# Optimization experiments

Measured on AMD Instinct MI355X. Metric: run time of the kernel, lower is better.

Reference implementation:

```python
import jax, jax.numpy as jnp
import numpy as np

N = 100000      # nodes
E = 1600000     # directed edges (avg degree 16)
D_IN = 64
D_OUT = 64


def setup_inputs() -> dict:
    key = jax.random.key(0)
    k1, k2, k3, k4, k5 = jax.random.split(key, 5)
    x = jax.random.normal(k1, (N, D_IN), dtype=jnp.float32)
    edge_index = jax.random.randint(k2, (2, E), 0, N, dtype=jnp.int32)
    s_in = 1.0 / np.sqrt(D_IN)
    W_conv = jax.random.normal(k3, (D_IN, D_OUT), dtype=jnp.float32) * s_in
    b_conv = jnp.zeros((D_OUT,), dtype=jnp.float32)
    W_self = jax.random.normal(k4, (D_IN, D_OUT), dtype=jnp.float32) * s_in
    b_self = jax.random.normal(k5, (D_OUT,), dtype=jnp.float32) * s_in
    return {"x": x, "edge_index": edge_index, "W_conv": W_conv, "b_conv": b_conv,
            "W_self": W_self, "b_self": b_self, "n1": 400, "n2": 250}


def reference(x, edge_index, W_conv, b_conv, W_self, b_self, n1, n2):
    # GCNConv (PyG defaults): add self-loops, symmetric normalization,
    # out_i = sum_j norm_ij * (x_j @ W_conv) + b_conv; then self-loop linear + residual.
    n = x.shape[0]
    loops = jnp.arange(n, dtype=edge_index.dtype)
    row = jnp.concatenate([edge_index[0], loops])  # source nodes [E+N]
    col = jnp.concatenate([edge_index[1], loops])  # target nodes [E+N]
    deg = jax.ops.segment_sum(jnp.ones_like(col, dtype=x.dtype), col, num_segments=n)
    dinv = jnp.where(deg > 0, jax.lax.rsqrt(deg), 0.0)      # deg^{-1/2}
    norm = dinv[row] * dinv[col]                            # [E+N]
    xw = x @ W_conv                                         # [N, D_OUT]
    msg = xw[row] * norm[:, None]                           # gather + scale [E+N, D_OUT]
    x_neigh = jax.ops.segment_sum(msg, col, num_segments=n) + b_conv
    x_self = x @ W_self + b_self
    return x_self + x_neigh
```

## Files before the change

kernel.cpp:

```cpp
#include <hip/hip_runtime.h>

#define CAP 64
#define CHUNK 4096
#define NBINS_MAX 1024
#define CAPB 2560

typedef __attribute__((ext_vector_type(8))) short bf16x8;
typedef __attribute__((ext_vector_type(4))) float f32x4;

__device__ __forceinline__ unsigned short f2bf_rne(float f) {
    unsigned u = __builtin_bit_cast(unsigned, f);
    u += 0x7FFFu + ((u >> 16) & 1u);
    return (unsigned short)(u >> 16);
}
__device__ __forceinline__ float bf2f(unsigned short h) {
    return __builtin_bit_cast(float, (unsigned)h << 16);
}


__global__ void k_zero2(int* __restrict__ gcur, int nbins, int* __restrict__ degovf,
                        int n, int* __restrict__ ovfc,
                        const float* __restrict__ Wc, const float* __restrict__ Ws,
                        unsigned short* __restrict__ bfrag) {
    const int t = threadIdx.x;
    if (blockIdx.x == gridDim.x - 1) {
        for (int s = t; s < 2048; s += 256) {
            int lane = s & 63;
            int ct   = (s >> 6) & 3;
            int ks   = (s >> 8) & 1;
            int half = (s >> 9) & 1;
            int mat  = (s >> 10) & 1;
            const float* W = mat ? Ws : Wc;
            int d = ct * 16 + (lane & 15);
            int kbase = ks * 32 + (lane >> 4) * 8;
#pragma unroll
            for (int j = 0; j < 8; ++j) {
                float v = W[(kbase + j) * 64 + d];
                unsigned u = __builtin_bit_cast(unsigned, v);
                unsigned short hi = (unsigned short)(u >> 16);
                unsigned short elem;
                if (half == 0) {
                    elem = hi;
                } else {
                    float fh = __builtin_bit_cast(float, (unsigned)hi << 16);
                    float fl = v - fh;
                    elem = (unsigned short)(__builtin_bit_cast(unsigned, fl) >> 16);
                }
                bfrag[(size_t)s * 8 + j] = elem;
            }
        }
        return;
    }
    int i = blockIdx.x * blockDim.x + t;
    if (i < nbins) gcur[i] = 0;
    if (i < n) degovf[i] = 0;
    if (i == 0) *ovfc = 0;
}

__global__ __launch_bounds__(512) void k_bin(
    const int* __restrict__ row, const int* __restrict__ col, int e, int nbins,
    int* __restrict__ gcur, unsigned int* __restrict__ records,
    int* __restrict__ degovf, int* __restrict__ ovf, int* __restrict__ ovfc)
{
    __shared__ int hist[NBINS_MAX];
    __shared__ int lofs[NBINS_MAX];
    __shared__ int gadj[NBINS_MAX];
    __shared__ int tscan[512];
    __shared__ unsigned int stage[CHUNK];
    __shared__ unsigned short sbin[CHUNK];

    const int t = threadIdx.x;
    const int base = blockIdx.x * CHUNK;
    int cnt = e - base; if (cnt > CHUNK) cnt = CHUNK;
    if (cnt <= 0) return;

    for (int i = t; i < nbins; i += 512) hist[i] = 0;
    __syncthreads();

    for (int k = t; k < cnt; k += 512) atomicAdd(&hist[col[base + k] >> 7], 1);
    __syncthreads();

    const int b0 = t * 2;
    int h0 = (b0 < nbins) ? hist[b0] : 0;
    int h1 = (b0 + 1 < nbins) ? hist[b0 + 1] : 0;
    int s = h0 + h1;
    tscan[t] = s;
    __syncthreads();
    for (int off = 1; off < 512; off <<= 1) {
        int v = (t >= off) ? tscan[t - off] : 0;
        __syncthreads();
        tscan[t] += v;
        __syncthreads();
    }
    const int tbase = tscan[t] - s;

    if (b0 < nbins) {
        int gb = h0 ? atomicAdd(&gcur[b0], h0) : 0;
        lofs[b0] = tbase; gadj[b0] = gb - tbase;
    }
    if (b0 + 1 < nbins) {
        int lb = tbase + h0;
        int gb = h1 ? atomicAdd(&gcur[b0 + 1], h1) : 0;
        lofs[b0 + 1] = lb; gadj[b0 + 1] = gb - lb;
    }
    __syncthreads();

    for (int k = t; k < cnt; k += 512) {
        int c = col[base + k];
        int r = row[base + k];
        int b = c >> 7;
        int slot = atomicAdd(&lofs[b], 1);
        stage[slot] = ((unsigned)r << 7) | (unsigned)(c & 127);
        sbin[slot] = (unsigned short)b;
    }
    __syncthreads();

    for (int k = t; k < cnt; k += 512) {
        unsigned rec = stage[k];
        int b = sbin[k];
        int g = gadj[b] + k;
        if (g < CAPB) {
            records[(size_t)b * CAPB + g] = rec;
        } else {
            int q = atomicAdd(ovfc, 1);
            int c = (b << 7) | (int)(rec & 127u);
            ovf[2 * q]     = (int)(rec >> 7);
            ovf[2 * q + 1] = c;
            atomicAdd(&degovf[c], 1);
        }
    }
}

__global__ __launch_bounds__(256) void k_dinv(
    const int* __restrict__ gcur, const unsigned int* __restrict__ records,
    const int* __restrict__ degovf, float* __restrict__ dinv, int n)
{
    __shared__ int lh[128];
    const int b = blockIdx.x, t = threadIdx.x;
    if (t < 128) lh[t] = 0;
    __syncthreads();
    int m = gcur[b]; if (m > CAPB) m = CAPB;
    const unsigned int* rb = records + (size_t)b * CAPB;
    for (int k = t; k < m; k += 256) atomicAdd(&lh[rb[k] & 127u], 1);
    __syncthreads();
    if (t < 128) {
        int node = (b << 7) + t;
        if (node < n) dinv[node] = rsqrtf((float)(lh[t] + degovf[node] + 1));
    }
}

__global__ __launch_bounds__(256) void k_gemm5(
    const float* __restrict__ x, const unsigned short* __restrict__ bfrag,
    const float* __restrict__ bc, const float* __restrict__ bs,
    const float* __restrict__ dinv, unsigned short* __restrict__ ybf,
    float* __restrict__ out, int n)
{
    const int t = threadIdx.x;
    const int lane = t & 63;
    const int wid = t >> 6;
    const int rt0 = blockIdx.x * 128 + wid * 32;
    if (rt0 >= n) return;

    const int arow = lane & 15;
    const int kgrp = lane >> 4;

    bf16x8 a_hi[2][2], a_lo[2][2];
#pragma unroll
    for (int rt = 0; rt < 2; ++rt) {
        int row = rt0 + rt * 16 + arow;
        if (row >= n) row = n - 1;
        const float* xp = x + (size_t)row * 64 + kgrp * 8;
#pragma unroll
        for (int ks = 0; ks < 2; ++ks) {
            float4 f0 = *(const float4*)(xp + ks * 32);
            float4 f1 = *(const float4*)(xp + ks * 32 + 4);
            float f[8] = {f0.x, f0.y, f0.z, f0.w, f1.x, f1.y, f1.z, f1.w};
            bf16x8 h, l;
#pragma unroll
            for (int j = 0; j < 8; ++j) {
                unsigned u = __builtin_bit_cast(unsigned, f[j]);
                unsigned short hj = (unsigned short)(u >> 16);
                float fh = __builtin_bit_cast(float, (unsigned)hj << 16);
                float fl = f[j] - fh;
                unsigned short lj = (unsigned short)(__builtin_bit_cast(unsigned, fl) >> 16);
                h[j] = (short)hj;
                l[j] = (short)lj;
            }
            a_hi[rt][ks] = h;
            a_lo[rt][ks] = l;
        }
    }

    f32x4 acc[2][2][4];
#pragma unroll
    for (int m = 0; m < 2; ++m)
#pragma unroll
        for (int rt = 0; rt < 2; ++rt)
#pragma unroll
            for (int ct = 0; ct < 4; ++ct)
                acc[m][rt][ct] = (f32x4){0.f, 0.f, 0.f, 0.f};

#pragma unroll
    for (int mat = 0; mat < 2; ++mat) {
#pragma unroll
        for (int ks = 0; ks < 2; ++ks) {
#pragma unroll
            for (int ct = 0; ct < 4; ++ct) {
                const bf16x8 bh = *(const bf16x8*)(bfrag + ((size_t)((((mat * 2 + 0) * 2 + ks) * 4 + ct) * 64 + lane)) * 8);
                const bf16x8 bl = *(const bf16x8*)(bfrag + ((size_t)((((mat * 2 + 1) * 2 + ks) * 4 + ct) * 64 + lane)) * 8);
#pragma unroll
                for (int rt = 0; rt < 2; ++rt) {
                    acc[mat][rt][ct] = __builtin_amdgcn_mfma_f32_16x16x32_bf16(a_hi[rt][ks], bh, acc[mat][rt][ct], 0, 0, 0);
                    acc[mat][rt][ct] = __builtin_amdgcn_mfma_f32_16x16x32_bf16(a_lo[rt][ks], bh, acc[mat][rt][ct], 0, 0, 0);
                    acc[mat][rt][ct] = __builtin_amdgcn_mfma_f32_16x16x32_bf16(a_hi[rt][ks], bl, acc[mat][rt][ct], 0, 0, 0);
                }
            }
        }
    }

    const int dcol = lane & 15;
    const int rbase = (lane >> 4) * 4;
    float di[2][4];
#pragma unroll
    for (int rt = 0; rt < 2; ++rt)
#pragma unroll
        for (int reg = 0; reg < 4; ++reg) {
            int row = rt0 + rt * 16 + rbase + reg;
            di[rt][reg] = dinv[(row < n) ? row : (n - 1)];
        }

#pragma unroll
    for (int ct = 0; ct < 4; ++ct) {
        int d = ct * 16 + dcol;
        float bias = bc[d] + bs[d];
#pragma unroll
        for (int rt = 0; rt < 2; ++rt) {
#pragma unroll
            for (int reg = 0; reg < 4; ++reg) {
                int row = rt0 + rt * 16 + rbase + reg;
                if (row < n) {
                    float dv = di[rt][reg];
                    float zc = acc[0][rt][ct][reg];
                    ybf[(size_t)row * 64 + d] = f2bf_rne(zc * dv);
                    out[(size_t)row * 64 + d] = acc[1][rt][ct][reg] + bias + dv * dv * zc;
                }
            }
        }
    }
}

__global__ __launch_bounds__(512) void k_gather_bin4(
    const int* __restrict__ gcur, const unsigned int* __restrict__ records,
    const unsigned short* __restrict__ ybf, const float* __restrict__ dinv,
    float* __restrict__ out, int n)
{
    __shared__ unsigned int srec[CAPB];
    __shared__ int slist[CAPB];
    __shared__ int scnt[128];
    __shared__ int sinc[128];
    __shared__ int scur[128];

    const int b = blockIdx.x, t = threadIdx.x;
    int m = gcur[b]; if (m > CAPB) m = CAPB;

    if (t < 128) scnt[t] = 0;
    __syncthreads();

    for (int k = t; k < m; k += 512) {
        unsigned r = __builtin_nontemporal_load(&records[(size_t)b * CAPB + k]);
        srec[k] = r;
        atomicAdd(&scnt[r & 127u], 1);
    }
    __syncthreads();

    if (t < 128) sinc[t] = scnt[t];
    __syncthreads();
    for (int off = 1; off < 128; off <<= 1) {
        int v = 0;
        if (t < 128 && t >= off) v = sinc[t - off];
        __syncthreads();
        if (t < 128) sinc[t] += v;
        __syncthreads();
    }
    if (t < 128) scur[t] = sinc[t] - scnt[t];
    __syncthreads();

    for (int k = t; k < m; k += 512) {
        unsigned r = srec[k];
        int slot = atomicAdd(&scur[r & 127u], 1);
        slist[slot] = (int)(r & ~127u);
    }
    __syncthreads();

    const int wave = t >> 6, lane = t & 63;
    const int h = lane >> 5;
    const char* ybl = (const char*)ybf + ((lane & 31) << 2);

    for (int i = wave; i < 128; i += 8) {
        int node = (b << 7) + i;
        if (node >= n) break;
        int cnt = scnt[i];
        if (cnt == 0) continue;
        int beg = sinc[i] - cnt;
        float ax0=0.f,ax1=0.f,ax2=0.f,ax3=0.f,ax4=0.f,ax5=0.f,ax6=0.f,ax7=0.f;
        float ay0=0.f,ay1=0.f,ay2=0.f,ay3=0.f,ay4=0.f,ay5=0.f,ay6=0.f,ay7=0.f;
        int k = 0;
        for (; k + 16 <= cnt; k += 16) {
            int o0 = slist[beg + k + 0  + h];
            int o1 = slist[beg + k + 2  + h];
            int o2 = slist[beg + k + 4  + h];
            int o3 = slist[beg + k + 6  + h];
            int o4 = slist[beg + k + 8  + h];
            int o5 = slist[beg + k + 10 + h];
            int o6 = slist[beg + k + 12 + h];
            int o7 = slist[beg + k + 14 + h];
            unsigned v0 = *(const unsigned*)(ybl + o0);
            unsigned v1 = *(const unsigned*)(ybl + o1);
            unsigned v2 = *(const unsigned*)(ybl + o2);
            unsigned v3 = *(const unsigned*)(ybl + o3);
            unsigned v4 = *(const unsigned*)(ybl + o4);
            unsigned v5 = *(const unsigned*)(ybl + o5);
            unsigned v6 = *(const unsigned*)(ybl + o6);
            unsigned v7 = *(const unsigned*)(ybl + o7);
            ax0 += bf2f((unsigned short)v0); ay0 += bf2f((unsigned short)(v0 >> 16));
            ax1 += bf2f((unsigned short)v1); ay1 += bf2f((unsigned short)(v1 >> 16));
            ax2 += bf2f((unsigned short)v2); ay2 += bf2f((unsigned short)(v2 >> 16));
            ax3 += bf2f((unsigned short)v3); ay3 += bf2f((unsigned short)(v3 >> 16));
            ax4 += bf2f((unsigned short)v4); ay4 += bf2f((unsigned short)(v4 >> 16));
            ax5 += bf2f((unsigned short)v5); ay5 += bf2f((unsigned short)(v5 >> 16));
            ax6 += bf2f((unsigned short)v6); ay6 += bf2f((unsigned short)(v6 >> 16));
            ax7 += bf2f((unsigned short)v7); ay7 += bf2f((unsigned short)(v7 >> 16));
        }
        for (; k + 2 <= cnt; k += 2) {
            int o = slist[beg + k + h];
            unsigned v = *(const unsigned*)(ybl + o);
            ax0 += bf2f((unsigned short)v);
            ay0 += bf2f((unsigned short)(v >> 16));
        }
        if (k < cnt && h == 0) {
            int o = slist[beg + k];
            unsigned v = *(const unsigned*)(ybl + o);
            ax0 += bf2f((unsigned short)v);
            ay0 += bf2f((unsigned short)(v >> 16));
        }
        float sx = ((ax0+ax1)+(ax2+ax3)) + ((ax4+ax5)+(ax6+ax7));
        float sy = ((ay0+ay1)+(ay2+ay3)) + ((ay4+ay5)+(ay6+ay7));
        sx += __shfl_down(sx, 32);
        sy += __shfl_down(sy, 32);
        if (h == 0) {
            float dv = dinv[node];
            float* op = out + (size_t)node * 64 + ((lane & 31) << 1);
            float p0 = __builtin_nontemporal_load(op);
            float p1 = __builtin_nontemporal_load(op + 1);
            __builtin_nontemporal_store(p0 + dv * sx, op);
            __builtin_nontemporal_store(p1 + dv * sy, op + 1);
        }
    }
}

__global__ void k_ovf2(const int* __restrict__ ovfc, const int* __restrict__ ovf,
                       const float* __restrict__ dinv, const unsigned short* __restrict__ ybf,
                       float* __restrict__ out) {
    int m = *ovfc;
    long long total = (long long)m * 64;
    for (long long idx = blockIdx.x * blockDim.x + threadIdx.x; idx < total;
         idx += (long long)gridDim.x * blockDim.x) {
        int q = (int)(idx >> 6);
        int j = (int)(idx & 63);
        int r = ovf[2 * q], c = ovf[2 * q + 1];
        float s = dinv[c];
        float v = bf2f(ybf[(size_t)r * 64 + j]);
        unsafeAtomicAdd(out + (size_t)c * 64 + j, s * v);
    }
}


__global__ void k_init(int* __restrict__ cnt, int* __restrict__ ovf_cnt, int n) {
    int i = blockIdx.x * blockDim.x + threadIdx.x;
    if (i < n) cnt[i] = 0;
    if (i == 0) *ovf_cnt = 0;
}

__global__ void k_fill_pad(const int* __restrict__ row, const int* __restrict__ col,
                           int* __restrict__ cnt, int* __restrict__ bucket,
                           int* __restrict__ ovf, int* __restrict__ ovf_cnt, int e) {
    int i = blockIdx.x * blockDim.x + threadIdx.x;
    if (i >= e) return;
    int c = col[i];
    int p = atomicAdd(&cnt[c], 1);
    if (p < CAP) bucket[(size_t)c * CAP + p] = row[i];
    else { int q = atomicAdd(ovf_cnt, 1); ovf[q] = i; }
}

__global__ __launch_bounds__(256) void k_gemm(
    const float* __restrict__ x, const float* __restrict__ Wc,
    const float* __restrict__ bc, const float* __restrict__ Ws,
    const float* __restrict__ bs, const int* __restrict__ deg, int add,
    float* __restrict__ dinv, float* __restrict__ y,
    float* __restrict__ out, int n)
{
    __shared__ __align__(16) float sWc[64 * 64];
    __shared__ __align__(16) float sWs[64 * 64];
    __shared__ __align__(16) float sx[64 * 64];
    const int t = threadIdx.x;

    for (int i = t; i < 1024; i += 256) {
        ((float4*)sWc)[i] = ((const float4*)Wc)[i];
        ((float4*)sWs)[i] = ((const float4*)Ws)[i];
    }
    const int row0 = blockIdx.x * 64;
    int nrows = n - row0; if (nrows > 64) nrows = 64;
    for (int i = t; i < nrows * 16; i += 256) {
        ((float4*)sx)[i] = ((const float4*)(x + (size_t)row0 * 64))[i];
    }
    __syncthreads();

    const int d = t & 63;
    const int g = t >> 6;

    float wcr[64], wsr[64];
#pragma unroll
    for (int k = 0; k < 64; ++k) { wcr[k] = sWc[k * 64 + d]; wsr[k] = sWs[k * 64 + d]; }

    const float bcd = bc[d], bsd = bs[d];

    for (int rr = g * 16; rr < (g + 1) * 16; ++rr) {
        if (rr >= nrows) break;
        float accC = 0.f, accS = 0.f;
        const float4* xv4 = (const float4*)(sx + rr * 64);
#pragma unroll
        for (int q = 0; q < 16; ++q) {
            float4 xv = xv4[q];
            accC += xv.x*wcr[4*q+0] + xv.y*wcr[4*q+1] + xv.z*wcr[4*q+2] + xv.w*wcr[4*q+3];
            accS += xv.x*wsr[4*q+0] + xv.y*wsr[4*q+1] + xv.z*wsr[4*q+2] + xv.w*wsr[4*q+3];
        }
        const int r = row0 + rr;
        const float di = rsqrtf((float)(deg[r] + add));
        if (d == 0) dinv[r] = di;
        const float yv = accC * di;
        y[(size_t)r * 64 + d] = yv;
        out[(size_t)r * 64 + d] = accS + bsd + bcd + di * yv;
    }
}

__global__ __launch_bounds__(256) void k_gather_pad(
    const int* __restrict__ cnt, const int* __restrict__ bucket,
    const float* __restrict__ y, float* __restrict__ out, int n)
{
    const int node = blockIdx.x * 4 + (threadIdx.x >> 6);
    if (node >= n) return;
    const int lane = threadIdx.x & 63;
    int m = cnt[node];
    const float di = rsqrtf((float)(m + 1));
    if (m > CAP) m = CAP;
    if (m == 0) return;

    int rl = (lane < m) ? bucket[(size_t)node * CAP + lane] : 0;

    float a0=0.f,a1=0.f,a2=0.f,a3=0.f,a4=0.f,a5=0.f,a6=0.f,a7=0.f;
    int k = 0;
    for (; k + 8 <= m; k += 8) {
        int r0=__shfl(rl,k+0), r1=__shfl(rl,k+1), r2=__shfl(rl,k+2), r3=__shfl(rl,k+3);
        int r4=__shfl(rl,k+4), r5=__shfl(rl,k+5), r6=__shfl(rl,k+6), r7=__shfl(rl,k+7);
        a0 += y[(size_t)r0*64 + lane];
        a1 += y[(size_t)r1*64 + lane];
        a2 += y[(size_t)r2*64 + lane];
        a3 += y[(size_t)r3*64 + lane];
        a4 += y[(size_t)r4*64 + lane];
        a5 += y[(size_t)r5*64 + lane];
        a6 += y[(size_t)r6*64 + lane];
        a7 += y[(size_t)r7*64 + lane];
    }
    for (; k + 2 <= m; k += 2) {
        int r0=__shfl(rl,k+0), r1=__shfl(rl,k+1);
        a0 += y[(size_t)r0*64 + lane];
        a1 += y[(size_t)r1*64 + lane];
    }
    if (k < m) { int r0=__shfl(rl,k); a0 += y[(size_t)r0*64 + lane]; }

    float acc = ((a0+a1)+(a2+a3)) + ((a4+a5)+(a6+a7));
    out[(size_t)node*64 + lane] += di * acc;
}

__global__ void k_ovf_idx(const int* __restrict__ ovf_cnt, const int* __restrict__ ovf,
                          const int* __restrict__ row, const int* __restrict__ col,
                          const float* __restrict__ dinv, const float* __restrict__ y,
                          float* __restrict__ out) {
    int m = *ovf_cnt;
    long long total = (long long)m * 16;
    for (long long idx = blockIdx.x*blockDim.x+threadIdx.x; idx < total;
         idx += (long long)gridDim.x*blockDim.x) {
        int ei = ovf[idx >> 4];
        int j = (int)(idx & 15);
        int r = row[ei], c = col[ei];
        float s = dinv[c];
        float4 v = ((const float4*)y)[(size_t)r*16 + j];
        float* o = out + (size_t)c*64 + (j<<2);
        unsafeAtomicAdd(o+0, s*v.x);
        unsafeAtomicAdd(o+1, s*v.y);
        unsafeAtomicAdd(o+2, s*v.z);
        unsafeAtomicAdd(o+3, s*v.w);
    }
}

__global__ void k_deg_init(int* __restrict__ deg, int n) {
    int i = blockIdx.x * blockDim.x + threadIdx.x;
    if (i < n) deg[i] = 1;
}

__global__ void k_deg_count(const int* __restrict__ col, int* __restrict__ deg, int e) {
    int i = blockIdx.x * blockDim.x + threadIdx.x;
    if (i < e) atomicAdd(&deg[col[i]], 1);
}

__global__ __launch_bounds__(256) void k_scatter(
    const int* __restrict__ row, const int* __restrict__ col,
    const float* __restrict__ dinv, const float* __restrict__ y,
    float* __restrict__ out, int e)
{
    int idx = blockIdx.x * blockDim.x + threadIdx.x;
    int eidx = idx >> 4;
    if (eidx >= e) return;
    int j = idx & 15;
    int r = row[eidx];
    int c = col[eidx];
    float s = dinv[c];
    float4 v = ((const float4*)y)[(size_t)r * 16 + j];
    float* o = out + (size_t)c * 64 + (j << 2);
    unsafeAtomicAdd(o + 0, s * v.x);
    unsafeAtomicAdd(o + 1, s * v.y);
    unsafeAtomicAdd(o + 2, s * v.z);
    unsafeAtomicAdd(o + 3, s * v.w);
}

extern "C" void kernel_launch(void* const* d_in, const int* in_sizes, int n_in,
                              void* d_out, int out_size, void* d_ws, size_t ws_size,
                              hipStream_t stream) {
    const float* x  = (const float*)d_in[0];
    const int*   ei = (const int*)d_in[1];
    const float* Wc = (const float*)d_in[2];
    const float* bc = (const float*)d_in[3];
    const float* Ws = (const float*)d_in[4];
    const float* bs = (const float*)d_in[5];
    float* out = (float*)d_out;

    const int n = in_sizes[0] / 64;
    const int e = in_sizes[1] / 2;
    const int* rowi = ei;
    const int* coli = ei + e;

    auto align = [](size_t v) { return (v + 255) & ~(size_t)255; };
    char* ws = (char*)d_ws;
    const int nbins = (n + 127) >> 7;

    size_t m_dinv = 0;
    size_t m_y    = align(m_dinv + (size_t)n * 4);
    size_t m_gcur = align(m_y    + (size_t)n * 128);
    size_t m_rec  = align(m_gcur + (size_t)nbins * 4);
    size_t m_dov  = align(m_rec  + (size_t)nbins * CAPB * 4);
    size_t m_ovf  = align(m_dov  + (size_t)n * 4);
    size_t m_ovfc = align(m_ovf  + (size_t)e * 8);
    size_t m_bfr  = align(m_ovfc + 256);
    size_t m_tot  = m_bfr + 32768;

    size_t p_cnt  = 0;
    size_t p_dinv = align(p_cnt  + (size_t)n * 4);
    size_t p_y    = align(p_dinv + (size_t)n * 4);
    size_t p_bkt  = align(p_y    + (size_t)n * 256);
    size_t p_ovf  = align(p_bkt  + (size_t)n * CAP * 4);
    size_t p_ovfc = align(p_ovf  + (size_t)e * 4);
    size_t p_tot  = p_ovfc + 256;

    if (nbins <= NBINS_MAX && m_tot <= ws_size) {
        float* dinv = (float*)(ws + m_dinv);
        unsigned short* ybf = (unsigned short*)(ws + m_y);
        int*   gcur = (int*)(ws + m_gcur);
        unsigned int* rec = (unsigned int*)(ws + m_rec);
        int*   dov  = (int*)(ws + m_dov);
        int*   ovf  = (int*)(ws + m_ovf);
        int*   ovfc = (int*)(ws + m_ovfc);
        unsigned short* bfrag = (unsigned short*)(ws + m_bfr);

        int zmax = (n > nbins) ? n : nbins;
        k_zero2<<<(zmax + 255) / 256 + 1, 256, 0, stream>>>(gcur, nbins, dov, n, ovfc,
                                                            Wc, Ws, bfrag);
        k_bin<<<(e + CHUNK - 1) / CHUNK, 512, 0, stream>>>(rowi, coli, e, nbins,
                                                           gcur, rec, dov, ovf, ovfc);
        k_dinv<<<nbins, 256, 0, stream>>>(gcur, rec, dov, dinv, n);
        k_gemm5<<<(n + 127) / 128, 256, 0, stream>>>(x, bfrag, bc, bs, dinv, ybf, out, n);
        k_gather_bin4<<<nbins, 512, 0, stream>>>(gcur, rec, ybf, dinv, out, n);
        k_ovf2<<<64, 256, 0, stream>>>(ovfc, ovf, dinv, ybf, out);
    } else if (p_tot <= ws_size) {
        int*   cnt    = (int*)(ws + p_cnt);
        float* dinv   = (float*)(ws + p_dinv);
        float* y      = (float*)(ws + p_y);
        int*   bucket = (int*)(ws + p_bkt);
        int*   ovf    = (int*)(ws + p_ovf);
        int*   ovfc   = (int*)(ws + p_ovfc);

        k_init<<<(n + 255) / 256, 256, 0, stream>>>(cnt, ovfc, n);
        k_fill_pad<<<(e + 255) / 256, 256, 0, stream>>>(rowi, coli, cnt, bucket, ovf, ovfc, e);
        k_gemm<<<(n + 63) / 64, 256, 0, stream>>>(x, Wc, bc, Ws, bs, cnt, 1, dinv, y, out, n);
        k_gather_pad<<<(n + 3) / 4, 256, 0, stream>>>(cnt, bucket, y, out, n);
        k_ovf_idx<<<64, 256, 0, stream>>>(ovfc, ovf, rowi, coli, dinv, y, out);
    } else {
        size_t a_deg  = 0;
        size_t a_dinv = align(a_deg  + (size_t)n * 4);
        size_t a_y    = align(a_dinv + (size_t)n * 4);
        int*   deg  = (int*)(ws + a_deg);
        float* dinv = (float*)(ws + a_dinv);
        float* y    = (float*)(ws + a_y);
        k_deg_init<<<(n + 255) / 256, 256, 0, stream>>>(deg, n);
        k_deg_count<<<(e + 255) / 256, 256, 0, stream>>>(coli, deg, e);
        k_gemm<<<(n + 63) / 64, 256, 0, stream>>>(x, Wc, bc, Ws, bs, deg, 0, dinv, y, out, n);
        long long tot = (long long)e * 16;
        k_scatter<<<(int)((tot + 255) / 256), 256, 0, stream>>>(rowi, coli, dinv, y, out, e);
    }
}
```

Measured before the change: 115.4 us.

## Fuse degree-normalization into GEMM kernel and drop low-part correction MFMA

Merges the per-bin degree histogram and rsqrt computation into the GEMM kernel, so each 128-node block computes its dinv values into shared memory and uses them directly. This removes one kernel launch and the global dinv reload. It also drops the split-bf16 low-part term of x and truncates x to bf16, cutting MFMA count from three to two per tile. In exchange, precision of x@W is reduced, which may risk accuracy tolerance.

Result: no change. 113.9 us, median of 2 (-1.3%).

```diff
diff --git a/kernel.cpp b/kernel.cpp
--- a/kernel.cpp
+++ b/kernel.cpp
@@ -131,12 +131,19 @@
     }
 }
 
-__global__ __launch_bounds__(256) void k_dinv(
-    const int* __restrict__ gcur, const unsigned int* __restrict__ records,
-    const int* __restrict__ degovf, float* __restrict__ dinv, int n)
+__global__ __launch_bounds__(256) void k_gemm6(
+    const float* __restrict__ x, const unsigned short* __restrict__ bfrag,
+    const float* __restrict__ bc, const float* __restrict__ bs,
+    const unsigned int* __restrict__ records, const int* __restrict__ gcur,
+    const int* __restrict__ degovf, float* __restrict__ dinv,
+    unsigned short* __restrict__ ybf, float* __restrict__ out, int n)
 {
     __shared__ int lh[128];
-    const int b = blockIdx.x, t = threadIdx.x;
+    __shared__ float sdinv[128];
+
+    const int b = blockIdx.x;
+    const int t = threadIdx.x;
+
     if (t < 128) lh[t] = 0;
     __syncthreads();
     int m = gcur[b]; if (m > CAPB) m = CAPB;
@@ -145,26 +152,23 @@
     __syncthreads();
     if (t < 128) {
         int node = (b << 7) + t;
-        if (node < n) dinv[node] = rsqrtf((float)(lh[t] + degovf[node] + 1));
-    }
-}
-
-__global__ __launch_bounds__(256) void k_gemm5(
-    const float* __restrict__ x, const unsigned short* __restrict__ bfrag,
-    const float* __restrict__ bc, const float* __restrict__ bs,
-    const float* __restrict__ dinv, unsigned short* __restrict__ ybf,
-    float* __restrict__ out, int n)
-{
-    const int t = threadIdx.x;
+        int dov = (node < n) ? degovf[node] : 0;
+        float v = rsqrtf((float)(lh[t] + dov + 1));
+        sdinv[t] = v;
+        if (node < n) dinv[node] = v;
+    }
+    __syncthreads();
+
     const int lane = t & 63;
     const int wid = t >> 6;
-    const int rt0 = blockIdx.x * 128 + wid * 32;
+    const int rt0 = b * 128 + wid * 32;
+    const int lbase = wid * 32;
     if (rt0 >= n) return;
 
     const int arow = lane & 15;
     const int kgrp = lane >> 4;
 
-    bf16x8 a_hi[2][2], a_lo[2][2];
+    bf16x8 a_hi[2][2];
 #pragma unroll
     for (int rt = 0; rt < 2; ++rt) {
         int row = rt0 + rt * 16 + arow;
@@ -175,30 +179,24 @@
             float4 f0 = *(const float4*)(xp + ks * 32);
             float4 f1 = *(const float4*)(xp + ks * 32 + 4);
             float f[8] = {f0.x, f0.y, f0.z, f0.w, f1.x, f1.y, f1.z, f1.w};
-            bf16x8 h, l;
+            bf16x8 h;
 #pragma unroll
             for (int j = 0; j < 8; ++j) {
                 unsigned u = __builtin_bit_cast(unsigned, f[j]);
-                unsigned short hj = (unsigned short)(u >> 16);
-                float fh = __builtin_bit_cast(float, (unsigned)hj << 16);
-                float fl = f[j] - fh;
-                unsigned short lj = (unsigned short)(__builtin_bit_cast(unsigned, fl) >> 16);
-                h[j] = (short)hj;
-                l[j] = (short)lj;
+                h[j] = (short)(unsigned short)(u >> 16);
             }
             a_hi[rt][ks] = h;
-            a_lo[rt][ks] = l;
         }
     }
 
     f32x4 acc[2][2][4];
 #pragma unroll
-    for (int m = 0; m < 2; ++m)
+    for (int mm = 0; mm < 2; ++mm)
 #pragma unroll
         for (int rt = 0; rt < 2; ++rt)
 #pragma unroll
             for (int ct = 0; ct < 4; ++ct)
-                acc[m][rt][ct] = (f32x4){0.f, 0.f, 0.f, 0.f};
+                acc[mm][rt][ct] = (f32x4){0.f, 0.f, 0.f, 0.f};
 
 #pragma unroll
     for (int mat = 0; mat < 2; ++mat) {
@@ -211,7 +209,6 @@
 #pragma unroll
                 for (int rt = 0; rt < 2; ++rt) {
                     acc[mat][rt][ct] = __builtin_amdgcn_mfma_f32_16x16x32_bf16(a_hi[rt][ks], bh, acc[mat][rt][ct], 0, 0, 0);
-                    acc[mat][rt][ct] = __builtin_amdgcn_mfma_f32_16x16x32_bf16(a_lo[rt][ks], bh, acc[mat][rt][ct], 0, 0, 0);
                     acc[mat][rt][ct] = __builtin_amdgcn_mfma_f32_16x16x32_bf16(a_hi[rt][ks], bl, acc[mat][rt][ct], 0, 0, 0);
                 }
             }
@@ -224,10 +221,8 @@
 #pragma unroll
     for (int rt = 0; rt < 2; ++rt)
 #pragma unroll
-        for (int reg = 0; reg < 4; ++reg) {
-            int row = rt0 + rt * 16 + rbase + reg;
-            di[rt][reg] = dinv[(row < n) ? row : (n - 1)];
-        }
+        for (int reg = 0; reg < 4; ++reg)
+            di[rt][reg] = sdinv[lbase + rt * 16 + rbase + reg];
 
 #pragma unroll
     for (int ct = 0; ct < 4; ++ct) {
@@ -586,8 +581,8 @@
                                                             Wc, Ws, bfrag);
         k_bin<<<(e + CHUNK - 1) / CHUNK, 512, 0, stream>>>(rowi, coli, e, nbins,
                                                            gcur, rec, dov, ovf, ovfc);
-        k_dinv<<<nbins, 256, 0, stream>>>(gcur, rec, dov, dinv, n);
-        k_gemm5<<<(n + 127) / 128, 256, 0, stream>>>(x, bfrag, bc, bs, dinv, ybf, out, n);
+        k_gemm6<<<nbins, 256, 0, stream>>>(x, bfrag, bc, bs, rec, gcur, dov,
+                                           dinv, ybf, out, n);
         k_gather_bin4<<<nbins, 512, 0, stream>>>(gcur, rec, ybf, dinv, out, n);
         k_ovf2<<<64, 256, 0, stream>>>(ovfc, ovf, dinv, ybf, out);
     } else if (p_tot <= ws_size) {
```
